# Kernel optimization log

Hardware: AMD Instinct MI355X
Metric: run time of the kernel (lower is better)

The kernel has to match this reference:

```python
import jax, jax.numpy as jnp
import numpy as np

B = 32          # number of trees (batch)
N_LEAVES = 512  # complete binary tree -> 2*N_LEAVES-1 nodes per tree
IN_DIM = 1024
MEM = 1024


def setup_inputs() -> dict:
    key = jax.random.key(0)
    k1, k2, k3, k4 = jax.random.split(key, 4)
    s = 0.02
    inputs = jax.random.normal(k1, (B, N_LEAVES, IN_DIM), jnp.float32)
    w_fioux = jax.random.normal(k2, (4 * MEM, IN_DIM), jnp.float32) * s
    # rand_init: bias zero except first mem_dim entries set to 1 (forget-gate bias)
    b_fioux = jnp.zeros((4 * MEM,), jnp.float32).at[:MEM].set(1.0)
    w_iouh = jax.random.normal(k3, (3 * MEM, 2 * MEM), jnp.float32) * s
    w_fh = jax.random.normal(k4, (2 * MEM, 2 * MEM), jnp.float32) * s
    return {"inputs": inputs, "w_fioux": w_fioux, "b_fioux": b_fioux,
            "w_iouh": w_iouh, "w_fh": w_fh}


def _node_forward(x, child_c, child_h, w_fioux, b_fioux, w_iouh, w_fh):
    # x: [B, n, IN_DIM]; child_c/child_h: [B, n, 2*MEM] (left || right)
    fioux = x @ w_fioux.T + b_fioux                      # [B, n, 4M]
    fx, ix, ox, ux = jnp.split(fioux, 4, axis=-1)        # each [B, n, M]
    ih, oh, uh = jnp.split(child_h @ w_iouh.T, 3, axis=-1)
    i = jax.nn.sigmoid(ix + ih)
    o = jax.nn.sigmoid(ox + oh)
    u = jnp.tanh(ux + uh)
    # f gates: fx repeated for both children + fh(child_h)
    f = jax.nn.sigmoid(jnp.concatenate([fx, fx], axis=-1) + child_h @ w_fh.T)
    fc = f * child_c                                     # [B, n, 2M]
    c = i * u + fc[..., :MEM] + fc[..., MEM:]            # sum over the 2 children
    h = o * jnp.tanh(c)
    return c, h


def reference(inputs, w_fioux, b_fioux, w_iouh, w_fh):
    # Leaves: x = word input, child states are zeros
    z = jnp.zeros((B, N_LEAVES, 2 * MEM), inputs.dtype)
    c, h = _node_forward(inputs, z, z, w_fioux, b_fioux, w_iouh, w_fh)
    n = N_LEAVES
    # Internal nodes, level by level (log2(N_LEAVES) fixed iterations):
    # x = zeros (internal nodes have no token input), children are adjacent pairs.
    while n > 1:
        n //= 2
        child_c = c.reshape(B, n, 2 * MEM)   # [left_c || right_c]
        child_h = h.reshape(B, n, 2 * MEM)
        x = jnp.zeros((B, n, IN_DIM), inputs.dtype)
        c, h = _node_forward(x, child_c, child_h, w_fioux, b_fioux, w_iouh, w_fh)
    return h[:, 0, :]  # root hidden state, [B, MEM]
```

## Files before the change

kernel.cpp:

```cpp
#include <hip/hip_runtime.h>
#include <cstdint>
#include <cstddef>


typedef __attribute__((ext_vector_type(8))) short bf16x8;
typedef __attribute__((ext_vector_type(4))) float f32x4;

__device__ __forceinline__ float sig_(float x) { return 1.0f / (1.0f + __expf(-x)); }

__device__ __forceinline__ unsigned short f2bf_(float x) {
    union { float f; uint32_t u; } v; v.f = x;
    uint32_t r = v.u + 0x7fffu + ((v.u >> 16) & 1u);
    return (unsigned short)(r >> 16);
}
__device__ __forceinline__ float bf2f_(unsigned short u) {
    union { uint32_t u; float f; } v; v.u = ((uint32_t)u) << 16; return v.f;
}

#define GL16(g, l) __builtin_amdgcn_global_load_lds( \
    (const __attribute__((address_space(1))) void*)(g), \
    (__attribute__((address_space(3))) void*)(l), 16, 0, 0)

__global__ __launch_bounds__(512, 2)
void gemm256(const unsigned short* __restrict__ A,
             const unsigned short* __restrict__ W,
             unsigned short* __restrict__ C, int M, int N, int lda, int Klen)
{
    __shared__ unsigned short lA[4 * 8192];
    __shared__ unsigned short lB[4 * 8192];

    const int gx = gridDim.x, gy = gridDim.y;
    int id = blockIdx.x + gx * (blockIdx.y + gy * blockIdx.z);
    {
        const int nwg = gx * gy * gridDim.z;
        const int q = nwg >> 3, r = nwg & 7, x = id & 7, i = id >> 3;
        id = (x < r ? x * (q + 1) : r * (q + 1) + (x - r) * q) + i;
    }
    const int bz  = id / (gx * gy);
    const int rem = id - bz * gx * gy;
    const int by  = rem / gx;
    const int bx  = rem - by * gx;

    const int tid = threadIdx.x;
    const int ln  = tid & 63;
    const int wv  = tid >> 6;
    const int wrp = wv >> 2;
    const int wcp = wv & 3;
    const int row0 = by * 256;
    const int colb = bx * 256;
    const int kbase = bz * Klen;
    C += (size_t)bz * M * N;

    const int rowS = tid >> 2;
    const int gS   = (tid & 3) ^ ((tid >> 3) & 3);
    const unsigned short* a0 = A + (size_t)min(row0 + rowS,       M - 1) * lda + kbase + gS * 8;
    const unsigned short* a1 = A + (size_t)min(row0 + rowS + 128, M - 1) * lda + kbase + gS * 8;
    const unsigned short* b0 = W + (size_t)(colb + rowS)       * lda + kbase + gS * 8;
    const unsigned short* b1 = W + (size_t)(colb + rowS + 128) * lda + kbase + gS * 8;
    const int ld0 = tid * 8;
    const int ld1 = tid * 8 + 4096;

    int offA[8], offB[4];
    #pragma unroll
    for (int i = 0; i < 8; ++i) {
        const int r = wrp * 128 + i * 16 + (ln & 15);
        offA[i] = r * 32 + ((ln >> 4) ^ ((r >> 1) & 3)) * 8;
    }
    #pragma unroll
    for (int i = 0; i < 4; ++i) {
        const int r = wcp * 64 + i * 16 + (ln & 15);
        offB[i] = r * 32 + ((ln >> 4) ^ ((r >> 1) & 3)) * 8;
    }

    f32x4 acc[8][4] = {};
    const int P = Klen >> 5;

#define ISSUE_KH(kh) do { \
    const int _sl = (kh) & 3; \
    const size_t _ko = (size_t)(kh) * 32; \
    GL16(a0 + _ko, lA + _sl * 8192 + ld0); \
    GL16(a1 + _ko, lA + _sl * 8192 + ld1); \
    GL16(b0 + _ko, lB + _sl * 8192 + ld0); \
    GL16(b1 + _ko, lB + _sl * 8192 + ld1); \
} while (0)

    ISSUE_KH(0); ISSUE_KH(1); ISSUE_KH(2);
    asm volatile("s_waitcnt vmcnt(8)" ::: "memory");
    asm volatile("s_barrier" ::: "memory");

    for (int p = 0; p < P; ++p) {
        const unsigned short* pa = lA + (p & 3) * 8192;
        const unsigned short* pb = lB + (p & 3) * 8192;
        bf16x8 bf[4], af[4], ag[4];
        #pragma unroll
        for (int i = 0; i < 4; ++i) bf[i] = *(const bf16x8*)(pb + offB[i]);
        #pragma unroll
        for (int i = 0; i < 4; ++i) af[i] = *(const bf16x8*)(pa + offA[i]);
        #pragma unroll
        for (int i = 0; i < 4; ++i) ag[i] = *(const bf16x8*)(pa + offA[4 + i]);
        if (p <= P - 4) ISSUE_KH(p + 3);
        __builtin_amdgcn_s_setprio(1);
        #pragma unroll
        for (int m = 0; m < 4; ++m)
            #pragma unroll
            for (int n = 0; n < 4; ++n)
                acc[m][n] = __builtin_amdgcn_mfma_f32_16x16x32_bf16(af[m], bf[n], acc[m][n], 0, 0, 0);
        #pragma unroll
        for (int m = 0; m < 4; ++m)
            #pragma unroll
            for (int n = 0; n < 4; ++n)
                acc[4 + m][n] = __builtin_amdgcn_mfma_f32_16x16x32_bf16(ag[m], bf[n], acc[4 + m][n], 0, 0, 0);
        __builtin_amdgcn_s_setprio(0);
        if (p <= P - 4)      asm volatile("s_waitcnt vmcnt(8)" ::: "memory");
        else if (p == P - 3) asm volatile("s_waitcnt vmcnt(4)" ::: "memory");
        else if (p == P - 2) asm volatile("s_waitcnt vmcnt(0)" ::: "memory");
        if (p < P - 1) asm volatile("s_barrier" ::: "memory");
    }
#undef ISSUE_KH

    #pragma unroll
    for (int mi = 0; mi < 8; ++mi) {
        #pragma unroll
        for (int ni = 0; ni < 4; ++ni) {
            const int col = colb + wcp * 64 + ni * 16 + (ln & 15);
            #pragma unroll
            for (int rg = 0; rg < 4; ++rg) {
                const int r = row0 + wrp * 128 + mi * 16 + (ln >> 4) * 4 + rg;
                if (r < M) C[(size_t)r * N + col] = f2bf_(acc[mi][ni][rg]);
            }
        }
    }
}

__global__ __launch_bounds__(512, 2)
void gemm320f(const unsigned short* __restrict__ A,
              const unsigned short* __restrict__ Wp,
              const float* __restrict__ b,
              const unsigned short* __restrict__ c_prev,
              unsigned short* __restrict__ c_out,
              unsigned short* __restrict__ h_out,
              int M)
{
    __shared__ unsigned short lA[4 * 8192];
    __shared__ unsigned short lB[4 * 10240];
    const int lda = 2048;

    const int gx = gridDim.x, gy = gridDim.y;
    int id = blockIdx.x + gx * blockIdx.y;
    {
        const int nwg = gx * gy;
        const int q = nwg >> 3, r = nwg & 7, x = id & 7, i = id >> 3;
        id = (x < r ? x * (q + 1) : r * (q + 1) + (x - r) * q) + i;
    }
    const int by = id / gx;
    const int bx = id - by * gx;

    const int tid = threadIdx.x;
    const int ln  = tid & 63;
    const int wv  = tid >> 6;
    const int wrp = wv >> 2;
    const int wcp = wv & 3;
    const int row0 = by * 256;
    const int colb = bx * 320;
    const bool five = (wv < 4);

    const int rowS = tid >> 2;
    const int gS   = (tid & 3) ^ ((tid >> 3) & 3);
    const unsigned short* a0 = A + (size_t)min(row0 + rowS,       M - 1) * lda + gS * 8;
    const unsigned short* a1 = A + (size_t)min(row0 + rowS + 128, M - 1) * lda + gS * 8;
    const unsigned short* w0 = Wp + (size_t)(colb + rowS)       * lda + gS * 8;
    const unsigned short* w1 = Wp + (size_t)(colb + rowS + 128) * lda + gS * 8;
    const unsigned short* w2 = Wp + (size_t)(colb + 256 + ((tid & 255) >> 2)) * lda + gS * 8;
    const int ld0 = tid * 8;
    const int ld1 = tid * 8 + 4096;
    const int ld2 = (tid & 255) * 8 + 8192;

    int offA[8], offB[5];
    #pragma unroll
    for (int i = 0; i < 8; ++i) {
        const int r = wrp * 128 + i * 16 + (ln & 15);
        offA[i] = r * 32 + ((ln >> 4) ^ ((r >> 1) & 3)) * 8;
    }
    #pragma unroll
    for (int g = 0; g < 5; ++g) {
        const int r = g * 64 + wcp * 16 + (ln & 15);
        offB[g] = r * 32 + ((ln >> 4) ^ ((r >> 1) & 3)) * 8;
    }

    f32x4 acc[8][5] = {};
    const int P = 64;

#define ISSUE_F(kh) do { \
    const int _sl = (kh) & 3; \
    const size_t _ko = (size_t)(kh) * 32; \
    GL16(a0 + _ko, lA + _sl * 8192 + ld0); \
    GL16(a1 + _ko, lA + _sl * 8192 + ld1); \
    GL16(w0 + _ko, lB + _sl * 10240 + ld0); \
    GL16(w1 + _ko, lB + _sl * 10240 + ld1); \
    if (five) GL16(w2 + _ko, lB + _sl * 10240 + ld2); \
} while (0)

    ISSUE_F(0); ISSUE_F(1); ISSUE_F(2);
    if (five) asm volatile("s_waitcnt vmcnt(10)" ::: "memory");
    else      asm volatile("s_waitcnt vmcnt(8)"  ::: "memory");
    asm volatile("s_barrier" ::: "memory");

    for (int p = 0; p < P; ++p) {
        const unsigned short* pa = lA + (p & 3) * 8192;
        const unsigned short* pb = lB + (p & 3) * 10240;
        bf16x8 bf[5], af[4], ag[4];
        #pragma unroll
        for (int g = 0; g < 5; ++g) bf[g] = *(const bf16x8*)(pb + offB[g]);
        #pragma unroll
        for (int i = 0; i < 4; ++i) af[i] = *(const bf16x8*)(pa + offA[i]);
        #pragma unroll
        for (int i = 0; i < 4; ++i) ag[i] = *(const bf16x8*)(pa + offA[4 + i]);
        if (p <= P - 4) ISSUE_F(p + 3);
        __builtin_amdgcn_s_setprio(1);
        #pragma unroll
        for (int m = 0; m < 4; ++m)
            #pragma unroll
            for (int g = 0; g < 5; ++g)
                acc[m][g] = __builtin_amdgcn_mfma_f32_16x16x32_bf16(af[m], bf[g], acc[m][g], 0, 0, 0);
        #pragma unroll
        for (int m = 0; m < 4; ++m)
            #pragma unroll
            for (int g = 0; g < 5; ++g)
                acc[4 + m][g] = __builtin_amdgcn_mfma_f32_16x16x32_bf16(ag[m], bf[g], acc[4 + m][g], 0, 0, 0);
        __builtin_amdgcn_s_setprio(0);
        if (p <= P - 4) {
            if (five) asm volatile("s_waitcnt vmcnt(10)" ::: "memory");
            else      asm volatile("s_waitcnt vmcnt(8)"  ::: "memory");
        } else if (p == P - 3) {
            if (five) asm volatile("s_waitcnt vmcnt(5)" ::: "memory");
            else      asm volatile("s_waitcnt vmcnt(4)" ::: "memory");
        } else if (p == P - 2) {
            asm volatile("s_waitcnt vmcnt(0)" ::: "memory");
        }
        if (p < P - 1) asm volatile("s_barrier" ::: "memory");
    }
#undef ISSUE_F

    const int jg = bx * 64 + wcp * 16 + (ln & 15);
    const float bi = b[1024 + jg];
    const float bo = b[2048 + jg];
    const float bu = b[3072 + jg];
    const float bff = b[jg];
    #pragma unroll
    for (int mi = 0; mi < 8; ++mi) {
        #pragma unroll
        for (int rg = 0; rg < 4; ++rg) {
            const int r = row0 + wrp * 128 + mi * 16 + (ln >> 4) * 4 + rg;
            if (r < M) {
                const float cl = bf2f_(c_prev[(size_t)r * 2048 + jg]);
                const float cr = bf2f_(c_prev[(size_t)r * 2048 + 1024 + jg]);
                const float iv = sig_(acc[mi][0][rg] + bi);
                const float ov = sig_(acc[mi][1][rg] + bo);
                const float uv = tanhf(acc[mi][2][rg] + bu);
                const float flv = sig_(acc[mi][3][rg] + bff);
                const float frv = sig_(acc[mi][4][rg] + bff);
                const float c = iv * uv + flv * cl + frv * cr;
                const float h = ov * tanhf(c);
                c_out[(size_t)r * 1024 + jg] = f2bf_(c);
                h_out[(size_t)r * 1024 + jg] = f2bf_(h);
            }
        }
    }
}

__global__ void f2bf_vec(const float* __restrict__ src, unsigned short* __restrict__ dst, int n4)
{
    const int i = blockIdx.x * blockDim.x + threadIdx.x;
    if (i >= n4) return;
    const float4 v = ((const float4*)src)[i];
    ushort4 o;
    o.x = f2bf_(v.x); o.y = f2bf_(v.y); o.z = f2bf_(v.z); o.w = f2bf_(v.w);
    ((ushort4*)dst)[i] = o;
}

__global__ void build_wcatp(const float* __restrict__ w_iouh, const float* __restrict__ w_fh,
                            unsigned short* __restrict__ dst, int total4)
{
    const int idx = blockIdx.x * blockDim.x + threadIdx.x;
    if (idx >= total4) return;
    const int rp = idx >> 9;
    const int c4 = (idx & 511) << 2;
    const int t  = rp / 320;
    const int q  = rp - t * 320;
    const int g  = q >> 6;
    const int jj = q & 63;
    const int srow = t * 64 + jj;
    const float* src = (g < 3) ? (w_iouh + (size_t)(g * 1024 + srow) * 2048)
                               : (w_fh   + (size_t)((g - 3) * 1024 + srow) * 2048);
    const float4 v = *(const float4*)(src + c4);
    ushort4 o;
    o.x = f2bf_(v.x); o.y = f2bf_(v.y); o.z = f2bf_(v.z); o.w = f2bf_(v.w);
    *(ushort4*)(dst + (size_t)rp * 2048 + c4) = o;
}

__global__ void leaf_gates(const unsigned short* __restrict__ g, const float* __restrict__ b,
                           unsigned short* __restrict__ c_out, unsigned short* __restrict__ h_out,
                           int rows)
{
    const int idx = blockIdx.x * blockDim.x + threadIdx.x;
    if (idx >= rows * 256) return;
    const int r = idx >> 8, q = (idx & 255) << 2;
    const unsigned short* gr = g + (size_t)r * 3072;
    const ushort4 ix = *(const ushort4*)(gr + q);
    const ushort4 ox = *(const ushort4*)(gr + 1024 + q);
    const ushort4 ux = *(const ushort4*)(gr + 2048 + q);
    const float* bi = b + 1024 + q;
    const float* bo = b + 2048 + q;
    const float* bu = b + 3072 + q;
    ushort4 co, ho;
    const float c0 = sig_(bf2f_(ix.x) + bi[0]) * tanhf(bf2f_(ux.x) + bu[0]);
    const float c1 = sig_(bf2f_(ix.y) + bi[1]) * tanhf(bf2f_(ux.y) + bu[1]);
    const float c2 = sig_(bf2f_(ix.z) + bi[2]) * tanhf(bf2f_(ux.z) + bu[2]);
    const float c3 = sig_(bf2f_(ix.w) + bi[3]) * tanhf(bf2f_(ux.w) + bu[3]);
    co.x = f2bf_(c0); co.y = f2bf_(c1); co.z = f2bf_(c2); co.w = f2bf_(c3);
    ho.x = f2bf_(sig_(bf2f_(ox.x) + bo[0]) * tanhf(c0));
    ho.y = f2bf_(sig_(bf2f_(ox.y) + bo[1]) * tanhf(c1));
    ho.z = f2bf_(sig_(bf2f_(ox.z) + bo[2]) * tanhf(c2));
    ho.w = f2bf_(sig_(bf2f_(ox.w) + bo[3]) * tanhf(c3));
    *(ushort4*)(c_out + (size_t)r * 1024 + q) = co;
    *(ushort4*)(h_out + (size_t)r * 1024 + q) = ho;
}

__device__ __forceinline__ void acc4_(float* v, ushort4 u) {
    v[0] += bf2f_(u.x); v[1] += bf2f_(u.y); v[2] += bf2f_(u.z); v[3] += bf2f_(u.w);
}

__global__ void node_gates(const unsigned short* __restrict__ g, int S, size_t sstride,
                           const float* __restrict__ b,
                           const unsigned short* __restrict__ c_prev,
                           unsigned short* __restrict__ c_out,
                           unsigned short* __restrict__ h_bf,
                           float* __restrict__ h_f32, int rows)
{
    const int idx = blockIdx.x * blockDim.x + threadIdx.x;
    if (idx >= rows * 256) return;
    const int r = idx >> 8, q = (idx & 255) << 2;
    const int t = q >> 6, jj = q & 63;
    float vi[4] = {}, vo[4] = {}, vu[4] = {}, vfl[4] = {}, vfr[4] = {};
    const unsigned short* gr = g + (size_t)r * 5120 + t * 320 + jj;
    for (int s = 0; s < S; ++s, gr += sstride) {
        acc4_(vi,  *(const ushort4*)(gr));
        acc4_(vo,  *(const ushort4*)(gr + 64));
        acc4_(vu,  *(const ushort4*)(gr + 128));
        acc4_(vfl, *(const ushort4*)(gr + 192));
        acc4_(vfr, *(const ushort4*)(gr + 256));
    }
    const float* bi = b + 1024 + q;
    const float* bo = b + 2048 + q;
    const float* bu = b + 3072 + q;
    const float* bff = b + q;
    const ushort4 clu = *(const ushort4*)(c_prev + (size_t)r * 2048 + q);
    const ushort4 cru = *(const ushort4*)(c_prev + (size_t)r * 2048 + 1024 + q);
    const float cl[4] = { bf2f_(clu.x), bf2f_(clu.y), bf2f_(clu.z), bf2f_(clu.w) };
    const float cr[4] = { bf2f_(cru.x), bf2f_(cru.y), bf2f_(cru.z), bf2f_(cru.w) };

    ushort4 co, ho;
    float cv[4], hv[4];
    #pragma unroll
    for (int e = 0; e < 4; ++e) {
        const float c = sig_(vi[e] + bi[e]) * tanhf(vu[e] + bu[e])
                      + sig_(vfl[e] + bff[e]) * cl[e]
                      + sig_(vfr[e] + bff[e]) * cr[e];
        cv[e] = c;
        hv[e] = sig_(vo[e] + bo[e]) * tanhf(c);
    }
    co.x = f2bf_(cv[0]); co.y = f2bf_(cv[1]); co.z = f2bf_(cv[2]); co.w = f2bf_(cv[3]);
    ho.x = f2bf_(hv[0]); ho.y = f2bf_(hv[1]); ho.z = f2bf_(hv[2]); ho.w = f2bf_(hv[3]);
    *(ushort4*)(c_out + (size_t)r * 1024 + q) = co;
    *(ushort4*)(h_bf + (size_t)r * 1024 + q) = ho;
    if (h_f32) {
        float4 hf; hf.x = hv[0]; hf.y = hv[1]; hf.z = hv[2]; hf.w = hv[3];
        *(float4*)(h_f32 + (size_t)r * 1024 + q) = hf;
    }
}

extern "C" void kernel_launch(void* const* d_in, const int* in_sizes, int n_in,
                              void* d_out, int out_size, void* d_ws, size_t ws_size,
                              hipStream_t stream)
{
    const float* inputs  = (const float*)d_in[0];
    const float* w_fioux = (const float*)d_in[1];
    const float* b_fioux = (const float*)d_in[2];
    const float* w_iouh  = (const float*)d_in[3];
    const float* w_fh    = (const float*)d_in[4];
    float* out = (float*)d_out;

    unsigned short* us    = (unsigned short*)d_ws;
    unsigned short* c_a   = us;
    unsigned short* c_b   = c_a + (size_t)16777216;
    unsigned short* h_a   = c_b + (size_t)8388608;
    unsigned short* h_b   = h_a + (size_t)16777216;
    unsigned short* wfx   = h_b + (size_t)8388608;
    unsigned short* wcatP = wfx + (size_t)3145728;
    unsigned short* gbuf  = wcatP + (size_t)10485760;
    unsigned short* x_bf  = c_a;

    f2bf_vec<<<16384, 256, 0, stream>>>(inputs, x_bf, 4194304);
    f2bf_vec<<<3072, 256, 0, stream>>>(w_fioux + (size_t)1024 * 1024, wfx, 786432);
    build_wcatp<<<10240, 256, 0, stream>>>(w_iouh, w_fh, wcatP, 5120 * 512);

    gemm256<<<dim3(12, 64, 1), 512, 0, stream>>>(x_bf, wfx, gbuf, 16384, 3072, 1024, 1024);
    leaf_gates<<<16384, 256, 0, stream>>>(gbuf, b_fioux, c_a, h_a, 16384);

    unsigned short *hp = h_a, *cp = c_a, *hn = h_b, *cn = c_b;
    for (int n = 256; n >= 64; n >>= 1) {
        const int m = 32 * n;
        gemm320f<<<dim3(16, m / 256), 512, 0, stream>>>(hp, wcatP, b_fioux, cp, cn, hn, m);
        unsigned short* t;
        t = hp; hp = hn; hn = t;
        t = cp; cp = cn; cn = t;
    }

    for (int n = 32; n >= 1; n >>= 1) {
        const int m = 32 * n;
        const int S = (m >= 512) ? 4 : 8;
        const int Klen = 2048 / S;
        gemm256<<<dim3(20, (m + 255) / 256, S), 512, 0, stream>>>(
            hp, wcatP, gbuf, m, 5120, 2048, Klen);
        node_gates<<<m, 256, 0, stream>>>(
            gbuf, S, (size_t)m * 5120, b_fioux, cp, cn, hn,
            (n == 1) ? out : nullptr, m);
        unsigned short* t;
        t = hp; hp = hn; hn = t;
        t = cp; cp = cn; cn = t;
    }
    (void)in_sizes; (void)n_in; (void)out_size; (void)ws_size;
}
```

Before: 708.0 us.

## Fuse leaf gate activations into leaf GEMM with permuted weight layout

Replaces the leaf-level GEMM plus separate leaf_gates kernel with a fused gemm384f kernel. The i/o/u input weights are permuted so each 384-column tile holds matching gate columns, and the gate nonlinearities are computed in the epilogue, writing c and h directly. This removes the round trip of the 16384x3072 gate buffer through global memory and one kernel launch. The tile shape changes to 128x384, which alters reuse and occupancy. The gemm320f block-to-XCD remapping is also simplified to a fixed swizzle.

```diff
diff --git a/kernel.cpp b/kernel.cpp
--- a/kernel.cpp
+++ b/kernel.cpp
@@ -22,111 +22,109 @@
     (__attribute__((address_space(3))) void*)(l), 16, 0, 0)
 
 __global__ __launch_bounds__(512, 2)
-void gemm256(const unsigned short* __restrict__ A,
-             const unsigned short* __restrict__ W,
-             unsigned short* __restrict__ C, int M, int N, int lda, int Klen)
-{
-    __shared__ unsigned short lA[4 * 8192];
-    __shared__ unsigned short lB[4 * 8192];
-
-    const int gx = gridDim.x, gy = gridDim.y;
-    int id = blockIdx.x + gx * (blockIdx.y + gy * blockIdx.z);
-    {
-        const int nwg = gx * gy * gridDim.z;
-        const int q = nwg >> 3, r = nwg & 7, x = id & 7, i = id >> 3;
-        id = (x < r ? x * (q + 1) : r * (q + 1) + (x - r) * q) + i;
-    }
-    const int bz  = id / (gx * gy);
-    const int rem = id - bz * gx * gy;
-    const int by  = rem / gx;
-    const int bx  = rem - by * gx;
+void gemm384f(const unsigned short* __restrict__ A,
+              const unsigned short* __restrict__ Wp,
+              const float* __restrict__ b,
+              unsigned short* __restrict__ c_out,
+              unsigned short* __restrict__ h_out,
+              int M)
+{
+    __shared__ unsigned short lA[4 * 4096];
+    __shared__ unsigned short lB[4 * 12288];
+    const int lda = 1024;
+
+    const int orig = blockIdx.x + 8 * blockIdx.y;
+    const int bx = orig & 7;
+    const int by = orig >> 3;
 
     const int tid = threadIdx.x;
     const int ln  = tid & 63;
     const int wv  = tid >> 6;
     const int wrp = wv >> 2;
     const int wcp = wv & 3;
-    const int row0 = by * 256;
-    const int colb = bx * 256;
-    const int kbase = bz * Klen;
-    C += (size_t)bz * M * N;
+    const int row0 = by * 128;
+    const int colb = bx * 384;
 
     const int rowS = tid >> 2;
     const int gS   = (tid & 3) ^ ((tid >> 3) & 3);
-    const unsigned short* a0 = A + (size_t)min(row0 + rowS,       M - 1) * lda + kbase + gS * 8;
-    const unsigned short* a1 = A + (size_t)min(row0 + rowS + 128, M - 1) * lda + kbase + gS * 8;
-    const unsigned short* b0 = W + (size_t)(colb + rowS)       * lda + kbase + gS * 8;
-    const unsigned short* b1 = W + (size_t)(colb + rowS + 128) * lda + kbase + gS * 8;
+    const unsigned short* a0 = A + (size_t)min(row0 + rowS, M - 1) * lda + gS * 8;
+    const unsigned short* w0 = Wp + (size_t)(colb + rowS)       * lda + gS * 8;
+    const unsigned short* w1 = Wp + (size_t)(colb + rowS + 128) * lda + gS * 8;
+    const unsigned short* w2 = Wp + (size_t)(colb + rowS + 256) * lda + gS * 8;
     const int ld0 = tid * 8;
     const int ld1 = tid * 8 + 4096;
-
-    int offA[8], offB[4];
-    #pragma unroll
-    for (int i = 0; i < 8; ++i) {
-        const int r = wrp * 128 + i * 16 + (ln & 15);
+    const int ld2 = tid * 8 + 8192;
+
+    int offA[4], offB[6];
+    #pragma unroll
+    for (int i = 0; i < 4; ++i) {
+        const int r = wrp * 64 + i * 16 + (ln & 15);
         offA[i] = r * 32 + ((ln >> 4) ^ ((r >> 1) & 3)) * 8;
     }
     #pragma unroll
-    for (int i = 0; i < 4; ++i) {
-        const int r = wcp * 64 + i * 16 + (ln & 15);
-        offB[i] = r * 32 + ((ln >> 4) ^ ((r >> 1) & 3)) * 8;
-    }
-
-    f32x4 acc[8][4] = {};
-    const int P = Klen >> 5;
-
-#define ISSUE_KH(kh) do { \
+    for (int h = 0; h < 2; ++h)
+        #pragma unroll
+        for (int g = 0; g < 3; ++g) {
+            const int r = h * 192 + g * 64 + wcp * 16 + (ln & 15);
+            offB[h * 3 + g] = r * 32 + ((ln >> 4) ^ ((r >> 1) & 3)) * 8;
+        }
+
+    f32x4 acc[4][6] = {};
+    const int P = 32;
+
+#define ISSUE_L(kh) do { \
     const int _sl = (kh) & 3; \
     const size_t _ko = (size_t)(kh) * 32; \
-    GL16(a0 + _ko, lA + _sl * 8192 + ld0); \
-    GL16(a1 + _ko, lA + _sl * 8192 + ld1); \
-    GL16(b0 + _ko, lB + _sl * 8192 + ld0); \
-    GL16(b1 + _ko, lB + _sl * 8192 + ld1); \
+    GL16(a0 + _ko, lA + _sl * 4096 + ld0); \
+    GL16(w0 + _ko, lB + _sl * 12288 + ld0); \
+    GL16(w1 + _ko, lB + _sl * 12288 + ld1); \
+    GL16(w2 + _ko, lB + _sl * 12288 + ld2); \
 } while (0)
 
-    ISSUE_KH(0); ISSUE_KH(1); ISSUE_KH(2);
+    ISSUE_L(0); ISSUE_L(1); ISSUE_L(2);
     asm volatile("s_waitcnt vmcnt(8)" ::: "memory");
     asm volatile("s_barrier" ::: "memory");
 
     for (int p = 0; p < P; ++p) {
-        const unsigned short* pa = lA + (p & 3) * 8192;
-        const unsigned short* pb = lB + (p & 3) * 8192;
-        bf16x8 bf[4], af[4], ag[4];
-        #pragma unroll
-        for (int i = 0; i < 4; ++i) bf[i] = *(const bf16x8*)(pb + offB[i]);
+        const unsigned short* pa = lA + (p & 3) * 4096;
+        const unsigned short* pb = lB + (p & 3) * 12288;
+        bf16x8 bf[6], af[4];
+        #pragma unroll
+        for (int i = 0; i < 6; ++i) bf[i] = *(const bf16x8*)(pb + offB[i]);
         #pragma unroll
         for (int i = 0; i < 4; ++i) af[i] = *(const bf16x8*)(pa + offA[i]);
-        #pragma unroll
-        for (int i = 0; i < 4; ++i) ag[i] = *(const bf16x8*)(pa + offA[4 + i]);
-        if (p <= P - 4) ISSUE_KH(p + 3);
+        if (p <= P - 4) ISSUE_L(p + 3);
         __builtin_amdgcn_s_setprio(1);
         #pragma unroll
         for (int m = 0; m < 4; ++m)
             #pragma unroll
-            for (int n = 0; n < 4; ++n)
-                acc[m][n] = __builtin_amdgcn_mfma_f32_16x16x32_bf16(af[m], bf[n], acc[m][n], 0, 0, 0);
-        #pragma unroll
-        for (int m = 0; m < 4; ++m)
-            #pragma unroll
-            for (int n = 0; n < 4; ++n)
-                acc[4 + m][n] = __builtin_amdgcn_mfma_f32_16x16x32_bf16(ag[m], bf[n], acc[4 + m][n], 0, 0, 0);
+            for (int g = 0; g < 6; ++g)
+                acc[m][g] = __builtin_amdgcn_mfma_f32_16x16x32_bf16(af[m], bf[g], acc[m][g], 0, 0, 0);
         __builtin_amdgcn_s_setprio(0);
         if (p <= P - 4)      asm volatile("s_waitcnt vmcnt(8)" ::: "memory");
         else if (p == P - 3) asm volatile("s_waitcnt vmcnt(4)" ::: "memory");
         else if (p == P - 2) asm volatile("s_waitcnt vmcnt(0)" ::: "memory");
         if (p < P - 1) asm volatile("s_barrier" ::: "memory");
     }
-#undef ISSUE_KH
-
-    #pragma unroll
-    for (int mi = 0; mi < 8; ++mi) {
-        #pragma unroll
-        for (int ni = 0; ni < 4; ++ni) {
-            const int col = colb + wcp * 64 + ni * 16 + (ln & 15);
+#undef ISSUE_L
+
+    #pragma unroll
+    for (int h = 0; h < 2; ++h) {
+        const int j = bx * 128 + h * 64 + wcp * 16 + (ln & 15);
+        const float bi = b[1024 + j];
+        const float bo = b[2048 + j];
+        const float bu = b[3072 + j];
+        #pragma unroll
+        for (int mi = 0; mi < 4; ++mi) {
             #pragma unroll
             for (int rg = 0; rg < 4; ++rg) {
-                const int r = row0 + wrp * 128 + mi * 16 + (ln >> 4) * 4 + rg;
-                if (r < M) C[(size_t)r * N + col] = f2bf_(acc[mi][ni][rg]);
+                const int r = row0 + wrp * 64 + mi * 16 + (ln >> 4) * 4 + rg;
+                if (r < M) {
+                    const float cv = sig_(acc[mi][h * 3 + 0][rg] + bi) * tanhf(acc[mi][h * 3 + 2][rg] + bu);
+                    const float hv = sig_(acc[mi][h * 3 + 1][rg] + bo) * tanhf(cv);
+                    c_out[(size_t)r * 1024 + j] = f2bf_(cv);
+                    h_out[(size_t)r * 1024 + j] = f2bf_(hv);
+                }
             }
         }
     }
@@ -145,15 +143,11 @@
     __shared__ unsigned short lB[4 * 10240];
     const int lda = 2048;
 
-    const int gx = gridDim.x, gy = gridDim.y;
-    int id = blockIdx.x + gx * blockIdx.y;
-    {
-        const int nwg = gx * gy;
-        const int q = nwg >> 3, r = nwg & 7, x = id & 7, i = id >> 3;
-        id = (x < r ? x * (q + 1) : r * (q + 1) + (x - r) * q) + i;
-    }
-    const int by = id / gx;
-    const int bx = id - by * gx;
+    const int orig = blockIdx.x + 16 * blockIdx.y;
+    const int xcd  = orig & 7;
+    const int pos  = orig >> 3;
+    const int bx   = xcd * 2 + (pos & 1);
+    const int by   = pos >> 1;
 
     const int tid = threadIdx.x;
     const int ln  = tid & 63;
@@ -268,6 +262,117 @@
     }
 }
 
+__global__ __launch_bounds__(512, 2)
+void gemm256(const unsigned short* __restrict__ A,
+             const unsigned short* __restrict__ W,
+             unsigned short* __restrict__ C, int M, int N, int lda, int Klen)
+{
+    __shared__ unsigned short lA[4 * 8192];
+    __shared__ unsigned short lB[4 * 8192];
+
+    const int gx = gridDim.x, gy = gridDim.y;
+    int id = blockIdx.x + gx * (blockIdx.y + gy * blockIdx.z);
+    {
+        const int nwg = gx * gy * gridDim.z;
+        const int q = nwg >> 3, r = nwg & 7, x = id & 7, i = id >> 3;
+        id = (x < r ? x * (q + 1) : r * (q + 1) + (x - r) * q) + i;
+    }
+    const int bz  = id / (gx * gy);
+    const int rem = id - bz * gx * gy;
+    const int by  = rem / gx;
+    const int bx  = rem - by * gx;
+
+    const int tid = threadIdx.x;
+    const int ln  = tid & 63;
+    const int wv  = tid >> 6;
+    const int wrp = wv >> 2;
+    const int wcp = wv & 3;
+    const int row0 = by * 256;
+    const int colb = bx * 256;
+    const int kbase = bz * Klen;
+    C += (size_t)bz * M * N;
+
+    const int rowS = tid >> 2;
+    const int gS   = (tid & 3) ^ ((tid >> 3) & 3);
+    const unsigned short* a0 = A + (size_t)min(row0 + rowS,       M - 1) * lda + kbase + gS * 8;
+    const unsigned short* a1 = A + (size_t)min(row0 + rowS + 128, M - 1) * lda + kbase + gS * 8;
+    const unsigned short* b0 = W + (size_t)(colb + rowS)       * lda + kbase + gS * 8;
+    const unsigned short* b1 = W + (size_t)(colb + rowS + 128) * lda + kbase + gS * 8;
+    const int ld0 = tid * 8;
+    const int ld1 = tid * 8 + 4096;
+
+    int offA[8], offB[4];
+    #pragma unroll
+    for (int i = 0; i < 8; ++i) {
+        const int r = wrp * 128 + i * 16 + (ln & 15);
+        offA[i] = r * 32 + ((ln >> 4) ^ ((r >> 1) & 3)) * 8;
+    }
+    #pragma unroll
+    for (int i = 0; i < 4; ++i) {
+        const int r = wcp * 64 + i * 16 + (ln & 15);
+        offB[i] = r * 32 + ((ln >> 4) ^ ((r >> 1) & 3)) * 8;
+    }
+
+    f32x4 acc[8][4] = {};
+    const int P = Klen >> 5;
+
+#define ISSUE_KH(kh) do { \
+    const int _sl = (kh) & 3; \
+    const size_t _ko = (size_t)(kh) * 32; \
+    GL16(a0 + _ko, lA + _sl * 8192 + ld0); \
+    GL16(a1 + _ko, lA + _sl * 8192 + ld1); \
+    GL16(b0 + _ko, lB + _sl * 8192 + ld0); \
+    GL16(b1 + _ko, lB + _sl * 8192 + ld1); \
+} while (0)
+
+    ISSUE_KH(0); ISSUE_KH(1); ISSUE_KH(2);
+    asm volatile("s_waitcnt vmcnt(8)" ::: "memory");
+    asm volatile("s_barrier" ::: "memory");
+
+    for (int p = 0; p < P; ++p) {
+        const unsigned short* pa = lA + (p & 3) * 8192;
+        const unsigned short* pb = lB + (p & 3) * 8192;
+        bf16x8 bf[4], af[4], ag[4];
+        #pragma unroll
+        for (int i = 0; i < 4; ++i) bf[i] = *(const bf16x8*)(pb + offB[i]);
+        #pragma unroll
+        for (int i = 0; i < 4; ++i) af[i] = *(const bf16x8*)(pa + offA[i]);
+        #pragma unroll
+        for (int i = 0; i < 4; ++i) ag[i] = *(const bf16x8*)(pa + offA[4 + i]);
+        if (p <= P - 4) ISSUE_KH(p + 3);
+        __builtin_amdgcn_s_setprio(1);
+        #pragma unroll
+        for (int m = 0; m < 4; ++m)
+            #pragma unroll
+            for (int n = 0; n < 4; ++n)
+                acc[m][n] = __builtin_amdgcn_mfma_f32_16x16x32_bf16(af[m], bf[n], acc[m][n], 0, 0, 0);
+        #pragma unroll
+        for (int m = 0; m < 4; ++m)
+            #pragma unroll
+            for (int n = 0; n < 4; ++n)
+                acc[4 + m][n] = __builtin_amdgcn_mfma_f32_16x16x32_bf16(ag[m], bf[n], acc[4 + m][n], 0, 0, 0);
+        __builtin_amdgcn_s_setprio(0);
+        if (p <= P - 4)      asm volatile("s_waitcnt vmcnt(8)" ::: "memory");
+        else if (p == P - 3) asm volatile("s_waitcnt vmcnt(4)" ::: "memory");
+        else if (p == P - 2) asm volatile("s_waitcnt vmcnt(0)" ::: "memory");
+        if (p < P - 1) asm volatile("s_barrier" ::: "memory");
+    }
+#undef ISSUE_KH
+
+    #pragma unroll
+    for (int mi = 0; mi < 8; ++mi) {
+        #pragma unroll
+        for (int ni = 0; ni < 4; ++ni) {
+            const int col = colb + wcp * 64 + ni * 16 + (ln & 15);
+            #pragma unroll
+            for (int rg = 0; rg < 4; ++rg) {
+                const int r = row0 + wrp * 128 + mi * 16 + (ln >> 4) * 4 + rg;
+                if (r < M) C[(size_t)r * N + col] = f2bf_(acc[mi][ni][rg]);
+            }
+        }
+    }
+}
+
 __global__ void f2bf_vec(const float* __restrict__ src, unsigned short* __restrict__ dst, int n4)
 {
     const int i = blockIdx.x * blockDim.x + threadIdx.x;
@@ -276,6 +381,24 @@
     ushort4 o;
     o.x = f2bf_(v.x); o.y = f2bf_(v.y); o.z = f2bf_(v.z); o.w = f2bf_(v.w);
     ((ushort4*)dst)[i] = o;
+}
+
+__global__ void build_wfxp(const float* __restrict__ w_fioux,
+                           unsigned short* __restrict__ dst, int total4)
+{
+    const int idx = blockIdx.x * blockDim.x + threadIdx.x;
+    if (idx >= total4) return;
+    const int rp = idx >> 8;
+    const int c4 = (idx & 255) << 2;
+    const int t  = rp / 192;
+    const int q  = rp - t * 192;
+    const int g  = q >> 6;
+    const int jj = q & 63;
+    const float* src = w_fioux + (size_t)((g + 1) * 1024 + t * 64 + jj) * 1024;
+    const float4 v = *(const float4*)(src + c4);
+    ushort4 o;
+    o.x = f2bf_(v.x); o.y = f2bf_(v.y); o.z = f2bf_(v.z); o.w = f2bf_(v.w);
+    *(ushort4*)(dst + (size_t)rp * 1024 + c4) = o;
 }
 
 __global__ void build_wcatp(const float* __restrict__ w_iouh, const float* __restrict__ w_fh,
@@ -298,34 +421,6 @@
     *(ushort4*)(dst + (size_t)rp * 2048 + c4) = o;
 }
 
-__global__ void leaf_gates(const unsigned short* __restrict__ g, const float* __restrict__ b,
-                           unsigned short* __restrict__ c_out, unsigned short* __restrict__ h_out,
-                           int rows)
-{
-    const int idx = blockIdx.x * blockDim.x + threadIdx.x;
-    if (idx >= rows * 256) return;
-    const int r = idx >> 8, q = (idx & 255) << 2;
-    const unsigned short* gr = g + (size_t)r * 3072;
-    const ushort4 ix = *(const ushort4*)(gr + q);
-    const ushort4 ox = *(const ushort4*)(gr + 1024 + q);
-    const ushort4 ux = *(const ushort4*)(gr + 2048 + q);
-    const float* bi = b + 1024 + q;
-    const float* bo = b + 2048 + q;
-    const float* bu = b + 3072 + q;
-    ushort4 co, ho;
-    const float c0 = sig_(bf2f_(ix.x) + bi[0]) * tanhf(bf2f_(ux.x) + bu[0]);
-    const float c1 = sig_(bf2f_(ix.y) + bi[1]) * tanhf(bf2f_(ux.y) + bu[1]);
-    const float c2 = sig_(bf2f_(ix.z) + bi[2]) * tanhf(bf2f_(ux.z) + bu[2]);
-    const float c3 = sig_(bf2f_(ix.w) + bi[3]) * tanhf(bf2f_(ux.w) + bu[3]);
-    co.x = f2bf_(c0); co.y = f2bf_(c1); co.z = f2bf_(c2); co.w = f2bf_(c3);
-    ho.x = f2bf_(sig_(bf2f_(ox.x) + bo[0]) * tanhf(c0));
-    ho.y = f2bf_(sig_(bf2f_(ox.y) + bo[1]) * tanhf(c1));
-    ho.z = f2bf_(sig_(bf2f_(ox.z) + bo[2]) * tanhf(c2));
-    ho.w = f2bf_(sig_(bf2f_(ox.w) + bo[3]) * tanhf(c3));
-    *(ushort4*)(c_out + (size_t)r * 1024 + q) = co;
-    *(ushort4*)(h_out + (size_t)r * 1024 + q) = ho;
-}
-
 __device__ __forceinline__ void acc4_(float* v, ushort4 u) {
     v[0] += bf2f_(u.x); v[1] += bf2f_(u.y); v[2] += bf2f_(u.z); v[3] += bf2f_(u.w);
 }
@@ -395,17 +490,16 @@
     unsigned short* c_b   = c_a + (size_t)16777216;
     unsigned short* h_a   = c_b + (size_t)8388608;
     unsigned short* h_b   = h_a + (size_t)16777216;
-    unsigned short* wfx   = h_b + (size_t)8388608;
-    unsigned short* wcatP = wfx + (size_t)3145728;
+    unsigned short* wfxP  = h_b + (size_t)8388608;
+    unsigned short* wcatP = wfxP + (size_t)3145728;
     unsigned short* gbuf  = wcatP + (size_t)10485760;
-    unsigned short* x_bf  = c_a;
+    unsigned short* x_bf  = gbuf;
 
     f2bf_vec<<<16384, 256, 0, stream>>>(inputs, x_bf, 4194304);
-    f2bf_vec<<<3072, 256, 0, stream>>>(w_fioux + (size_t)1024 * 1024, wfx, 786432);
+    build_wfxp<<<3072, 256, 0, stream>>>(w_fioux, wfxP, 786432);
     build_wcatp<<<10240, 256, 0, stream>>>(w_iouh, w_fh, wcatP, 5120 * 512);
 
-    gemm256<<<dim3(12, 64, 1), 512, 0, stream>>>(x_bf, wfx, gbuf, 16384, 3072, 1024, 1024);
-    leaf_gates<<<16384, 256, 0, stream>>>(gbuf, b_fioux, c_a, h_a, 16384);
+    gemm384f<<<dim3(8, 128), 512, 0, stream>>>(x_bf, wfxP, b_fioux, c_a, h_a, 16384);
 
     unsigned short *hp = h_a, *cp = c_a, *hn = h_b, *cn = c_b;
     for (int n = 256; n >= 64; n >>= 1) {
```

Result: faster. 693.6 us (-2.0%).
